# Optimization experiments

Hardware: AMD Instinct MI355X
Metric: run time of the kernel (lower is better)

The kernel has to match this reference:

```python
import jax, jax.numpy as jnp
import numpy as np

B, S, E, H = 4, 1024, 768, 8
HD = E // H
FF = 4 * E
SCALING = HD ** -0.5


def _layernorm(x, g, b, eps=1e-5):
    m = jnp.mean(x, axis=-1, keepdims=True)
    v = jnp.var(x, axis=-1, keepdims=True)
    return (x - m) / jnp.sqrt(v + eps) * g + b


def setup_inputs() -> dict:
    key = jax.random.key(0)
    ks = jax.random.split(key, 12)
    w = lambda k, shp: (jax.random.normal(k, shp, jnp.float32) * 0.02)
    return {
        "x": jax.random.normal(ks[0], (B, S, E), jnp.float32),
        "dist_map": jax.random.uniform(ks[1], (B, H, S, S), jnp.float32),
        "mask": jnp.zeros((B, S), jnp.int32),
        "Wq": w(ks[2], (E, E)), "bq": jnp.zeros((E,), jnp.float32),
        "Wk": w(ks[3], (E, E)), "bk": jnp.zeros((E,), jnp.float32),
        "Wv": w(ks[4], (E, E)), "bv": jnp.zeros((E,), jnp.float32),
        "Wo": w(ks[5], (E, E)), "bo": jnp.zeros((E,), jnp.float32),
        "ln1_g": jnp.ones((E,), jnp.float32), "ln1_b": jnp.zeros((E,), jnp.float32),
        "W1": w(ks[6], (FF, E)), "b1": jnp.zeros((FF,), jnp.float32),
        "W2": w(ks[7], (E, FF)), "b2": jnp.zeros((E,), jnp.float32),
        "ln2_g": jnp.ones((E,), jnp.float32), "ln2_b": jnp.zeros((E,), jnp.float32),
    }


def reference(x, dist_map, mask, Wq, bq, Wk, bk, Wv, bv, Wo, bo,
              ln1_g, ln1_b, W1, b1, W2, b2, ln2_g, ln2_b):
    # --- attention residual block (pre-norm) ---
    h = _layernorm(x, ln1_g, ln1_b)
    # NOTE: torch does .view(B, H, S, HD) directly on [B, S, E] -> pure reshape, no transpose
    q = (h @ Wq.T + bq).reshape(B, H, S, HD)
    k = (h @ Wk.T + bk).reshape(B, H, S, HD)
    v = (h @ Wv.T + bv).reshape(B, H, S, HD)
    attn_weights = jnp.einsum("bhqd,bhkd->bhqk", q, k)
    pad = mask.astype(bool)[:, None, None, :]          # [B,1,1,S]
    attn_weights = jnp.where(pad, -10000.0, attn_weights)  # mask BEFORE scaling (as in source)
    probs = jax.nn.softmax(attn_weights * SCALING, axis=-1)
    probs = (probs + dist_map) * 0.5                   # post-softmax dist bias
    ctx = jnp.einsum("bhal,bhlv->bhav", probs, v)      # [B,H,S,HD]
    ctx = ctx.transpose(0, 2, 1, 3).reshape(B, S, E)
    x1 = x + (ctx @ Wo.T + bo)
    # --- FFN residual block (pre-norm) ---
    h2 = _layernorm(x1, ln2_g, ln2_b)
    ffn = jax.nn.gelu(h2 @ W1.T + b1, approximate=False) @ W2.T + b2
    out = x1 + ffn
    return out, probs
```

## Files before the change

kernel.cpp:

```cpp
#include <hip/hip_runtime.h>
#include <math.h>

typedef unsigned short u16;
typedef u16   u16x8  __attribute__((ext_vector_type(8)));
typedef u16   u16x4  __attribute__((ext_vector_type(4)));
typedef __bf16 bf16x8 __attribute__((ext_vector_type(8)));
typedef float f32x4  __attribute__((ext_vector_type(4)));

#define SZ_BSE   3145728
#define HEADSZ   98304
#define SCALING  0.10206207261596577f

__device__ __forceinline__ u16 f2bf(float f) {
  union { float f; unsigned u; } c; c.f = f;
  unsigned u = c.u;
  return (u16)((u + 0x7fffu + ((u >> 16) & 1u)) >> 16);
}
__device__ __forceinline__ float bf2f(u16 v) {
  union { unsigned u; float f; } c; c.u = ((unsigned)v) << 16; return c.f;
}

typedef const __attribute__((address_space(1))) unsigned int* gas1_t;
typedef __attribute__((address_space(3))) unsigned int* las3_t;
__device__ __forceinline__ void gload16(const void* g, void* l) {
  __builtin_amdgcn_global_load_lds((gas1_t)g, (las3_t)l, 16, 0, 0);
}

struct CvtArgs {
  const float* src[6];
  u16* dst[6];
};
__global__ __launch_bounds__(256) void cvtall_k(CvtArgs a) {
  int bid = blockIdx.x;
  int which, base;
  if (bid < 2304)      { which = bid / 576; base = (bid - which * 576) * 1024; }
  else if (bid < 4608) { which = 4; base = (bid - 2304) * 1024; }
  else                 { which = 5; base = (bid - 4608) * 1024; }
  int i = base + threadIdx.x * 4;
  f32x4 v = *(const f32x4*)&a.src[which][i];
  u16x4 o; o[0]=f2bf(v[0]); o[1]=f2bf(v[1]); o[2]=f2bf(v[2]); o[3]=f2bf(v[3]);
  *(u16x4*)&a.dst[which][i] = o;
}

__global__ __launch_bounds__(256) void ln_k(const float* __restrict__ x,
                                            const float* __restrict__ g,
                                            const float* __restrict__ b,
                                            u16* __restrict__ out) {
  const int row = blockIdx.x;
  const float* xr = x + (long)row * 768;
  const int t = threadIdx.x;
  float v0 = xr[t], v1 = xr[t + 256], v2 = xr[t + 512];
  float s = v0 + v1 + v2, ss = v0*v0 + v1*v1 + v2*v2;
  for (int o = 32; o > 0; o >>= 1) { s += __shfl_xor(s, o); ss += __shfl_xor(ss, o); }
  __shared__ float red[8];
  int w = t >> 6;
  if ((t & 63) == 0) { red[w] = s; red[w + 4] = ss; }
  __syncthreads();
  s  = red[0] + red[1] + red[2] + red[3];
  ss = red[4] + red[5] + red[6] + red[7];
  float mean = s * (1.0f / 768.0f);
  float var  = ss * (1.0f / 768.0f) - mean * mean;
  float rstd = rsqrtf(var + 1e-5f);
  u16* orow = out + (long)row * 768;
  orow[t]       = f2bf((v0 - mean) * rstd * g[t]       + b[t]);
  orow[t + 256] = f2bf((v1 - mean) * rstd * g[t + 256] + b[t + 256]);
  orow[t + 512] = f2bf((v2 - mean) * rstd * g[t + 512] + b[t + 512]);
}

__global__ __launch_bounds__(256) void reduce_k(const float* __restrict__ p,
                                                const float* __restrict__ resid,
                                                const float* __restrict__ bias,
                                                float* __restrict__ out) {
  long i = ((long)blockIdx.x * 256 + threadIdx.x) * 4;
  f32x4 a = *(const f32x4*)&p[i];
  f32x4 b = *(const f32x4*)&p[3145728 + i];
  f32x4 c = *(const f32x4*)&p[6291456 + i];
  f32x4 r = *(const f32x4*)&resid[i];
  int cb = (int)(i % 768);
  f32x4 g = *(const f32x4*)&bias[cb];
  f32x4 o;
  o[0] = r[0] + g[0] + a[0] + b[0] + c[0];
  o[1] = r[1] + g[1] + a[1] + b[1] + c[1];
  o[2] = r[2] + g[2] + a[2] + b[2] + c[2];
  o[3] = r[3] + g[3] + a[3] + b[3] + c[3];
  *(f32x4*)&out[i] = o;
}

__global__ __launch_bounds__(512, 4)
void scores_k(const u16* __restrict__ qb, const u16* __restrict__ kb,
              const int* __restrict__ maskp, float* __restrict__ probs,
              float* __restrict__ rowsInv) {
  __shared__ u16 sP[8 * 16 * 72];
  __shared__ float sSum[2][64];
  __shared__ u16 sFlag[1024];

  const int t = threadIdx.x;
  const int z = blockIdx.y;
  const int r0 = blockIdx.x * 64;
  const int b = z >> 3;

  {
    const int* mp = maskp + b * 1024 + t * 2;
    int2 mv = *(const int2*)mp;
    sFlag[t * 2]     = (u16)(mv.x != 0);
    sFlag[t * 2 + 1] = (u16)(mv.y != 0);
  }
  __syncthreads();

  const int lane = t & 63;
  const int w = t >> 6;
  const int rs = w & 3, ch = w >> 2;
  const int wr0 = rs * 16;
  const int lr = lane & 15, lg = lane >> 4;
  const int cbase = ch * 512;
  u16* sPw = sP + w * (16 * 72);
  const int lrow = lane >> 2;
  const int cg = (lane & 3) * 16;

  const u16* qh = qb + (long)z * HEADSZ;
  const u16* kh = kb + (long)z * HEADSZ;
  u16* eb = (u16*)probs + (long)z * 2097152;

  bf16x8 qa[3];
  {
    const u16* qr = qh + (long)(r0 + wr0 + lr) * 96 + lg * 8;
#pragma unroll
    for (int kf = 0; kf < 3; ++kf) qa[kf] = *(const bf16x8*)(qr + kf * 32);
  }

  const float neg = -10000.0f * SCALING;
  float srun[4] = {0.f, 0.f, 0.f, 0.f};

  for (int c = 0; c < 8; ++c) {
    const int c0 = cbase + c * 64;
    f32x4 a4[4] = {};
#pragma unroll
    for (int ni = 0; ni < 4; ++ni) {
      const u16* kr = kh + (long)(c0 + ni * 16 + lr) * 96 + lg * 8;
#pragma unroll
      for (int kf = 0; kf < 3; ++kf)
        a4[ni] = __builtin_amdgcn_mfma_f32_16x16x32_bf16(
            qa[kf], *(const bf16x8*)(kr + kf * 32), a4[ni], 0, 0, 0);
    }
#pragma unroll
    for (int ni = 0; ni < 4; ++ni) {
      bool fm = sFlag[c0 + ni * 16 + lr] != 0;
#pragma unroll
      for (int r = 0; r < 4; ++r) {
        float sv = fm ? neg : a4[ni][r] * SCALING;
        float e = __expf(sv);
        srun[r] += e;
        sPw[(lg * 4 + r) * 72 + ni * 16 + lr] = f2bf(e);
      }
    }
    u16x8 e0 = *(const u16x8*)&sPw[lrow * 72 + cg];
    u16x8 e1 = *(const u16x8*)&sPw[lrow * 72 + cg + 8];
    u16* ep = eb + (long)(r0 + wr0 + lrow) * 2048 + 1024 + c0 + cg;
    *(u16x8*)ep       = e0;
    *(u16x8*)(ep + 8) = e1;
  }

#pragma unroll
  for (int r = 0; r < 4; ++r) {
    float s = srun[r];
    s += __shfl_xor(s, 1);
    s += __shfl_xor(s, 2);
    s += __shfl_xor(s, 4);
    s += __shfl_xor(s, 8);
    if (lr == 0) sSum[ch][wr0 + lg * 4 + r] = s;
  }
  __syncthreads();
  if (ch == 0 && lr == 0) {
#pragma unroll
    for (int r = 0; r < 4; ++r) {
      float iv = 1.0f / (sSum[0][wr0 + lg * 4 + r] + sSum[1][wr0 + lg * 4 + r]);
      rowsInv[(long)z * 1024 + r0 + wr0 + lg * 4 + r] = iv;
    }
  }
}

__global__ __launch_bounds__(256)
void probs_k(float* __restrict__ probs, const float* __restrict__ dist,
             const float* __restrict__ rowsInv) {
  const long gidx = (long)blockIdx.x * 4 + (threadIdx.x >> 6);
  const int l16 = (threadIdx.x & 63) * 16;
  float* pr = probs + gidx * 1024 + l16;
  const u16* er = (const u16*)(probs + gidx * 1024) + 1024 + l16;
  const float* dr = dist + gidx * 1024 + l16;
  const float iv = rowsInv[gidx];

  u16x8 e0 = *(const u16x8*)er;
  u16x8 e1 = *(const u16x8*)(er + 8);
  f32x4 d0 = *(const f32x4*)dr;
  f32x4 d1 = *(const f32x4*)(dr + 4);
  f32x4 d2 = *(const f32x4*)(dr + 8);
  f32x4 d3 = *(const f32x4*)(dr + 12);
  __syncthreads();
  f32x4 o0, o1, o2, o3;
#pragma unroll
  for (int j = 0; j < 4; ++j) {
    o0[j] = (bf2f(e0[j])     * iv + d0[j]) * 0.5f;
    o1[j] = (bf2f(e0[4 + j]) * iv + d1[j]) * 0.5f;
    o2[j] = (bf2f(e1[j])     * iv + d2[j]) * 0.5f;
    o3[j] = (bf2f(e1[4 + j]) * iv + d3[j]) * 0.5f;
  }
  *(f32x4*)pr        = o0;
  *(f32x4*)(pr + 4)  = o1;
  *(f32x4*)(pr + 8)  = o2;
  *(f32x4*)(pr + 12) = o3;
}

__global__ __launch_bounds__(512, 4)
void pv_k(const float* __restrict__ probs, const u16* __restrict__ vT,
          u16* __restrict__ ctx) {
  __shared__ float sX[4 * 64 * 24];
  const int t = threadIdx.x;
  const int z = blockIdx.y;
  const int r0 = blockIdx.x * 64;
  const int b = z >> 3, h = z & 7;
  const int lane = t & 63, w = t >> 6;
  const int rs = w & 3, kh = w >> 2;
  const int wr0 = rs * 16;
  const int lr = lane & 15, lg = lane >> 4;

  const float* ph = probs + (long)z * 1048576 + (long)(r0 + wr0 + lr) * 1024 + lg * 8;
  const u16* vh = vT + (long)z * HEADSZ;
  const int cb = kh * 512;

  f32x4 cacc[6] = {};
#pragma unroll
  for (int c = 0; c < 8; ++c) {
    const int c0 = cb + c * 64;
    const float* pp = ph + c0;
    f32x4 p0 = *(const f32x4*)pp;
    f32x4 p1 = *(const f32x4*)(pp + 4);
    f32x4 p2 = *(const f32x4*)(pp + 32);
    f32x4 p3 = *(const f32x4*)(pp + 36);
    u16x8 w0, w1;
#pragma unroll
    for (int j = 0; j < 4; ++j) {
      w0[j] = f2bf(p0[j]); w0[4 + j] = f2bf(p1[j]);
      w1[j] = f2bf(p2[j]); w1[4 + j] = f2bf(p3[j]);
    }
    bf16x8 pa0 = *(bf16x8*)&w0;
    bf16x8 pa1 = *(bf16x8*)&w1;
    const u16* vr0 = vh + (long)lr * 1024 + c0 + lg * 8;
#pragma unroll
    for (int n2 = 0; n2 < 6; ++n2) {
      bf16x8 vb = *(const bf16x8*)(vr0 + (long)n2 * 16384);
      cacc[n2] = __builtin_amdgcn_mfma_f32_16x16x32_bf16(pa0, vb, cacc[n2], 0, 0, 0);
    }
#pragma unroll
    for (int n2 = 0; n2 < 6; ++n2) {
      bf16x8 vb = *(const bf16x8*)(vr0 + 32 + (long)n2 * 16384);
      cacc[n2] = __builtin_amdgcn_mfma_f32_16x16x32_bf16(pa1, vb, cacc[n2], 0, 0, 0);
    }
  }

  __syncthreads();
  if (kh == 1) {
    float* xp = sX + ((rs * 64 + lane) * 24);
#pragma unroll
    for (int n2 = 0; n2 < 6; ++n2) *(f32x4*)&xp[n2 * 4] = cacc[n2];
  }
  __syncthreads();
  if (kh == 0) {
    const float* xp = sX + ((rs * 64 + lane) * 24);
    u16* cbp = ctx + (long)b * 786432 + h * 96;
#pragma unroll
    for (int n2 = 0; n2 < 6; ++n2) {
      f32x4 xv = *(const f32x4*)&xp[n2 * 4];
      int d = n2 * 16 + lr;
#pragma unroll
      for (int r = 0; r < 4; ++r)
        cbp[(long)(r0 + wr0 + lg * 4 + r) * 768 + d] = f2bf(cacc[n2][r] + xv[r]);
    }
  }
}

enum { EPI_QKV = 0, EPI_GELU = 1, EPI_PARTIAL = 2 };

template <int EPI>
__global__ __launch_bounds__(256, 2)
void gemm_k(const u16* __restrict__ A, int lda,
            const u16* __restrict__ W, int ldw,
            void* __restrict__ Cv, long sCz, int ldc,
            const float* __restrict__ bias,
            u16* __restrict__ vt,
            int N, int K, int kchunks) {
  __shared__ u16 sA[8192];
  __shared__ u16 sB[8192];

  const int t  = threadIdx.x;
  const int kc = blockIdx.z;
  const int klen = K / kchunks;
  const int kbeg = kc * klen, kend = kbeg + klen;
  const int m0 = blockIdx.x * 128;
  const int n0 = blockIdx.y * 128;

  const int r0 = t >> 2;
  const int c0 = (t & 3) << 3;
  char* lA = (char*)sA + ((t >> 6) << 10);
  char* lB = (char*)sB + ((t >> 6) << 10);

  const u16* gB0 = W + (long)(n0 + r0) * ldw + c0;
  const u16* gB1 = gB0 + 64 * ldw;
  const u16* gA0 = A + (long)(m0 + r0) * lda + c0;
  const u16* gA1 = gA0 + 64 * lda;

  const int lane = t & 63;
  const int w  = t >> 6;
  const int wm = (w >> 1) * 64, wn = (w & 1) * 64;
  const int lr = lane & 15, lg = lane >> 4;

  f32x4 acc[4][4] = {};

  for (int k0 = kbeg; k0 < kend; k0 += 64) {
    gload16(gA0 + k0,      lA);
    gload16(gA1 + k0,      lA + 4096);
    gload16(gA0 + k0 + 32, lA + 8192);
    gload16(gA1 + k0 + 32, lA + 12288);
    gload16(gB0 + k0,      lB);
    gload16(gB1 + k0,      lB + 4096);
    gload16(gB0 + k0 + 32, lB + 8192);
    gload16(gB1 + k0 + 32, lB + 12288);
    __syncthreads();

#pragma unroll
    for (int kk = 0; kk < 2; ++kk) {
      bf16x8 aF[4], bF[4];
#pragma unroll
      for (int mi = 0; mi < 4; ++mi)
        aF[mi] = *(const bf16x8*)&sA[kk * 4096 + (wm + mi * 16 + lr) * 32 + lg * 8];
#pragma unroll
      for (int ni = 0; ni < 4; ++ni)
        bF[ni] = *(const bf16x8*)&sB[kk * 4096 + (wn + ni * 16 + lr) * 32 + lg * 8];
#pragma unroll
      for (int mi = 0; mi < 4; ++mi)
#pragma unroll
        for (int ni = 0; ni < 4; ++ni)
          acc[mi][ni] = __builtin_amdgcn_mfma_f32_16x16x32_bf16(aF[mi], bF[ni], acc[mi][ni], 0, 0, 0);
    }
    __syncthreads();
  }

  long coff = (EPI == EPI_PARTIAL) ? (long)kc * sCz : 0;

#pragma unroll
  for (int mi = 0; mi < 4; ++mi) {
#pragma unroll
    for (int ni = 0; ni < 4; ++ni) {
      int gc = n0 + wn + ni * 16 + lr;
      int gr0 = m0 + wm + mi * 16 + lg * 4;
#pragma unroll
      for (int r = 0; r < 4; ++r) {
        float vv = acc[mi][ni][r];
        if (EPI == EPI_QKV) {
          vv += bias[gc];
          if (gc >= 1536) {
            int c = gc - 1536;
            int row = gr0 + r, bb = row >> 10, sr = row & 1023;
            int hh = sr >> 7;
            int cd = c / 96;
            int ss = ((sr & 127) << 3) + cd;
            int dd = c - cd * 96;
            vt[(long)(bb * 8 + hh) * HEADSZ + (long)dd * 1024 + ss] = f2bf(vv);
          } else {
            int wsel = gc >= 768 ? 1 : 0;
            int c = gc - wsel * 768;
            ((u16*)Cv)[(long)wsel * 3145728 + (long)(gr0 + r) * 768 + c] = f2bf(vv);
          }
        } else if (EPI == EPI_GELU) {
          vv += bias[gc];
          vv = 0.5f * vv * (1.0f + erff(vv * 0.70710678118654752f));
          ((u16*)Cv)[coff + (long)(gr0 + r) * ldc + gc] = f2bf(vv);
        } else {
          ((float*)Cv)[coff + (long)(gr0 + r) * ldc + gc] = vv;
        }
      }
    }
  }
}

extern "C" void kernel_launch(void* const* d_in, const int* in_sizes, int n_in,
                              void* d_out, int out_size, void* d_ws, size_t ws_size,
                              hipStream_t stream) {
  (void)in_sizes; (void)n_in; (void)out_size; (void)ws_size;
  const float* x    = (const float*)d_in[0];
  const float* dist = (const float*)d_in[1];
  const int*   mask = (const int*)d_in[2];
  const float* Wq = (const float*)d_in[3];  const float* bq  = (const float*)d_in[4];
  const float* Wk = (const float*)d_in[5];  const float* bk  = (const float*)d_in[6];
  const float* Wv = (const float*)d_in[7];  const float* bv  = (const float*)d_in[8];
  const float* Wo = (const float*)d_in[9];  const float* bo  = (const float*)d_in[10];
  const float* g1 = (const float*)d_in[11]; const float* b1n = (const float*)d_in[12];
  const float* W1 = (const float*)d_in[13]; const float* b1f = (const float*)d_in[14];
  const float* W2 = (const float*)d_in[15]; const float* b2f = (const float*)d_in[16];
  const float* g2 = (const float*)d_in[17]; const float* b2n = (const float*)d_in[18];

  char* ws = (char*)d_ws;
  u16*   h    = (u16*)(ws + 0);
  u16*   ctx  = (u16*)(ws + 0);
  u16*   qk   = (u16*)(ws + 6291456);
  u16*   q    = qk;
  u16*   k    = (u16*)(ws + 12582912);
  u16*   vT   = (u16*)(ws + 25165824);
  float* part = (float*)(ws + 6291456);
  u16*   h2   = (u16*)(ws + 31457280);
  u16*   ffn1 = (u16*)(ws + 44040192);
  float* x1   = (float*)(ws + 69206016);
  u16*   wqkvb= (u16*)(ws + 81788928);
  u16*   wob  = (u16*)(ws + 85327872);
  u16*   w1b  = (u16*)(ws + 86507520);
  u16*   w2b  = (u16*)(ws + 91226112);
  float* bqkv = (float*)(ws + 95944704);
  float* rowsInv = (float*)(ws + 95953920);

  float* outp   = (float*)d_out;
  float* probs  = outp + SZ_BSE;

  CvtArgs ca;
  ca.src[0] = Wq; ca.src[1] = Wk; ca.src[2] = Wv;
  ca.src[3] = Wo; ca.src[4] = W1; ca.src[5] = W2;
  ca.dst[0] = wqkvb; ca.dst[1] = wqkvb + 589824; ca.dst[2] = wqkvb + 1179648;
  ca.dst[3] = wob;   ca.dst[4] = w1b;            ca.dst[5] = w2b;
  cvtall_k<<<6912, 256, 0, stream>>>(ca);
  hipMemcpyAsync(bqkv,        bq, 3072, hipMemcpyDeviceToDevice, stream);
  hipMemcpyAsync(bqkv + 768,  bk, 3072, hipMemcpyDeviceToDevice, stream);
  hipMemcpyAsync(bqkv + 1536, bv, 3072, hipMemcpyDeviceToDevice, stream);

  ln_k<<<4096, 256, 0, stream>>>(x, g1, b1n, h);

  gemm_k<EPI_QKV><<<dim3(32, 18, 1), 256, 0, stream>>>(
      h, 768, wqkvb, 768, qk, 0, 768, bqkv, vT, 2304, 768, 1);

  scores_k<<<dim3(16, 32), 512, 0, stream>>>(q, k, mask, probs, rowsInv);
  probs_k<<<8192, 256, 0, stream>>>(probs, dist, rowsInv);
  pv_k<<<dim3(16, 32), 512, 0, stream>>>(probs, vT, ctx);

  gemm_k<EPI_PARTIAL><<<dim3(32, 6, 3), 256, 0, stream>>>(
      ctx, 768, wob, 768, part, 3145728, 768, nullptr, nullptr, 768, 768, 3);
  reduce_k<<<3072, 256, 0, stream>>>(part, x, bo, x1);

  ln_k<<<4096, 256, 0, stream>>>(x1, g2, b2n, h2);

  gemm_k<EPI_GELU><<<dim3(32, 24, 1), 256, 0, stream>>>(
      h2, 768, w1b, 768, ffn1, 0, 3072, b1f, nullptr, 3072, 768, 1);

  gemm_k<EPI_PARTIAL><<<dim3(32, 6, 3), 256, 0, stream>>>(
      ffn1, 3072, w2b, 3072, part, 3145728, 768, nullptr, nullptr, 768, 3072, 3);
  reduce_k<<<3072, 256, 0, stream>>>(part, x1, b2f, outp);
}
```

Baseline: 329.3 us.

## Fuse softmax normalization and dist bias into scores kernel, keep exps in registers

Merges the scores and probs kernels. Unnormalized bf16 exponentials are now held in registers across the whole 512-column chunk instead of being written to the probs buffer. After the row-sum reduction they are normalized, staged through LDS, combined with dist_map, and written once as fp32 probs. This removes the bf16 round trip through global memory and a kernel launch, at the cost of many extra registers (128 u16 values per thread) and larger shared memory, which may reduce occupancy.

New measurement: 377.7 us. 14.7% more time.

```diff
diff --git a/kernel.cpp b/kernel.cpp
--- a/kernel.cpp
+++ b/kernel.cpp
@@ -87,10 +87,10 @@
 }
 
 __global__ __launch_bounds__(512, 4)
-void scores_k(const u16* __restrict__ qb, const u16* __restrict__ kb,
-              const int* __restrict__ maskp, float* __restrict__ probs,
-              float* __restrict__ rowsInv) {
-  __shared__ u16 sP[8 * 16 * 72];
+void sp_k(const u16* __restrict__ qb, const u16* __restrict__ kb,
+          const int* __restrict__ maskp, const float* __restrict__ dist,
+          float* __restrict__ probs) {
+  __shared__ float sT[8][1088];
   __shared__ float sSum[2][64];
   __shared__ u16 sFlag[1024];
 
@@ -113,13 +113,12 @@
   const int wr0 = rs * 16;
   const int lr = lane & 15, lg = lane >> 4;
   const int cbase = ch * 512;
-  u16* sPw = sP + w * (16 * 72);
+  float* sTw = sT[w];
   const int lrow = lane >> 2;
   const int cg = (lane & 3) * 16;
 
   const u16* qh = qb + (long)z * HEADSZ;
   const u16* kh = kb + (long)z * HEADSZ;
-  u16* eb = (u16*)probs + (long)z * 2097152;
 
   bf16x8 qa[3];
   {
@@ -130,7 +129,9 @@
 
   const float neg = -10000.0f * SCALING;
   float srun[4] = {0.f, 0.f, 0.f, 0.f};
-
+  u16x4 eR[8][4];
+
+#pragma unroll
   for (int c = 0; c < 8; ++c) {
     const int c0 = cbase + c * 64;
     f32x4 a4[4] = {};
@@ -150,14 +151,9 @@
         float sv = fm ? neg : a4[ni][r] * SCALING;
         float e = __expf(sv);
         srun[r] += e;
-        sPw[(lg * 4 + r) * 72 + ni * 16 + lr] = f2bf(e);
+        eR[c][ni][r] = f2bf(e);
       }
     }
-    u16x8 e0 = *(const u16x8*)&sPw[lrow * 72 + cg];
-    u16x8 e1 = *(const u16x8*)&sPw[lrow * 72 + cg + 8];
-    u16* ep = eb + (long)(r0 + wr0 + lrow) * 2048 + 1024 + c0 + cg;
-    *(u16x8*)ep       = e0;
-    *(u16x8*)(ep + 8) = e1;
   }
 
 #pragma unroll
@@ -170,44 +166,45 @@
     if (lr == 0) sSum[ch][wr0 + lg * 4 + r] = s;
   }
   __syncthreads();
-  if (ch == 0 && lr == 0) {
-#pragma unroll
-    for (int r = 0; r < 4; ++r) {
-      float iv = 1.0f / (sSum[0][wr0 + lg * 4 + r] + sSum[1][wr0 + lg * 4 + r]);
-      rowsInv[(long)z * 1024 + r0 + wr0 + lg * 4 + r] = iv;
-    }
-  }
-}
-
-__global__ __launch_bounds__(256)
-void probs_k(float* __restrict__ probs, const float* __restrict__ dist,
-             const float* __restrict__ rowsInv) {
-  const long gidx = (long)blockIdx.x * 4 + (threadIdx.x >> 6);
-  const int l16 = (threadIdx.x & 63) * 16;
-  float* pr = probs + gidx * 1024 + l16;
-  const u16* er = (const u16*)(probs + gidx * 1024) + 1024 + l16;
-  const float* dr = dist + gidx * 1024 + l16;
-  const float iv = rowsInv[gidx];
-
-  u16x8 e0 = *(const u16x8*)er;
-  u16x8 e1 = *(const u16x8*)(er + 8);
-  f32x4 d0 = *(const f32x4*)dr;
-  f32x4 d1 = *(const f32x4*)(dr + 4);
-  f32x4 d2 = *(const f32x4*)(dr + 8);
-  f32x4 d3 = *(const f32x4*)(dr + 12);
-  __syncthreads();
-  f32x4 o0, o1, o2, o3;
-#pragma unroll
-  for (int j = 0; j < 4; ++j) {
-    o0[j] = (bf2f(e0[j])     * iv + d0[j]) * 0.5f;
-    o1[j] = (bf2f(e0[4 + j]) * iv + d1[j]) * 0.5f;
-    o2[j] = (bf2f(e1[j])     * iv + d2[j]) * 0.5f;
-    o3[j] = (bf2f(e1[4 + j]) * iv + d3[j]) * 0.5f;
-  }
-  *(f32x4*)pr        = o0;
-  *(f32x4*)(pr + 4)  = o1;
-  *(f32x4*)(pr + 8)  = o2;
-  *(f32x4*)(pr + 12) = o3;
+  float inv[4];
+#pragma unroll
+  for (int r = 0; r < 4; ++r)
+    inv[r] = 1.0f / (sSum[0][wr0 + lg * 4 + r] + sSum[1][wr0 + lg * 4 + r]);
+
+  const float* dh = dist + (long)z * 1048576;
+  float* ph = probs + (long)z * 1048576;
+#pragma unroll
+  for (int c = 0; c < 8; ++c) {
+    const int c0 = cbase + c * 64;
+#pragma unroll
+    for (int ni = 0; ni < 4; ++ni)
+#pragma unroll
+      for (int r = 0; r < 4; ++r)
+        sTw[(lg * 4 + r) * 68 + ni * 16 + lr] = bf2f(eR[c][ni][r]) * inv[r];
+    const float* sp = &sTw[lrow * 68 + cg];
+    f32x4 p0 = *(const f32x4*)sp;
+    f32x4 p1 = *(const f32x4*)(sp + 4);
+    f32x4 p2 = *(const f32x4*)(sp + 8);
+    f32x4 p3 = *(const f32x4*)(sp + 12);
+    const float* dp = dh + (long)(r0 + wr0 + lrow) * 1024 + c0 + cg;
+    float* pp = ph + (long)(r0 + wr0 + lrow) * 1024 + c0 + cg;
+    f32x4 d0 = *(const f32x4*)dp;
+    f32x4 d1 = *(const f32x4*)(dp + 4);
+    f32x4 d2 = *(const f32x4*)(dp + 8);
+    f32x4 d3 = *(const f32x4*)(dp + 12);
+    f32x4 o0, o1, o2, o3;
+#pragma unroll
+    for (int j = 0; j < 4; ++j) {
+      o0[j] = (p0[j] + d0[j]) * 0.5f;
+      o1[j] = (p1[j] + d1[j]) * 0.5f;
+      o2[j] = (p2[j] + d2[j]) * 0.5f;
+      o3[j] = (p3[j] + d3[j]) * 0.5f;
+    }
+    *(f32x4*)pp        = o0;
+    *(f32x4*)(pp + 4)  = o1;
+    *(f32x4*)(pp + 8)  = o2;
+    *(f32x4*)(pp + 12) = o3;
+  }
 }
 
 __global__ __launch_bounds__(512, 4)
@@ -414,7 +411,6 @@
   u16*   w1b  = (u16*)(ws + 86507520);
   u16*   w2b  = (u16*)(ws + 91226112);
   float* bqkv = (float*)(ws + 95944704);
-  float* rowsInv = (float*)(ws + 95953920);
 
   float* outp   = (float*)d_out;
   float* probs  = outp + SZ_BSE;
@@ -434,8 +430,7 @@
   gemm_k<EPI_QKV><<<dim3(32, 18, 1), 256, 0, stream>>>(
       h, 768, wqkvb, 768, qk, 0, 768, bqkv, vT, 2304, 768, 1);
 
-  scores_k<<<dim3(16, 32), 512, 0, stream>>>(q, k, mask, probs, rowsInv);
-  probs_k<<<8192, 256, 0, stream>>>(probs, dist, rowsInv);
+  sp_k<<<dim3(16, 32), 512, 0, stream>>>(q, k, mask, dist, probs);
   pv_k<<<dim3(16, 32), 512, 0, stream>>>(probs, vT, ctx);
 
   gemm_k<EPI_PARTIAL><<<dim3(32, 6, 3), 256, 0, stream>>>(
```
